# Kernel tuning notes

Measured on AMD Instinct MI355X. Metric: run time of the kernel, lower is better.

Reference implementation:

```python
import jax, jax.numpy as jnp
import numpy as np

N, E = 50000, 800000
IN_CH, N_HID, OUT_CH = 128, 256, 128
DROPOUT_P = 0.5


def gcn_conv(x, src, dst, ew, W, b, num_nodes):
    # PyG GCNConv with edge_weight: symmetric normalization with self-loops.
    loop = jnp.arange(num_nodes)
    s = jnp.concatenate([src, loop])
    d = jnp.concatenate([dst, loop])
    w = jnp.concatenate([ew, jnp.ones((num_nodes,), ew.dtype)])
    deg = jax.ops.segment_sum(w, d, num_segments=num_nodes)  # [N]
    dinv = jnp.where(deg > 0, jax.lax.rsqrt(deg), 0.0)
    norm = dinv[s] * w * dinv[d]                             # [E+N]
    h = x @ W                                                # [N, out]
    msg = h[s] * norm[:, None]                               # [E+N, out]
    out = jax.ops.segment_sum(msg, d, num_segments=num_nodes)
    return out + b


def setup_inputs() -> dict:
    key = jax.random.key(0)
    ks = jax.random.split(key, 8)
    x = jax.random.normal(ks[0], (N, IN_CH), dtype=jnp.float32)
    edge_index = jax.random.randint(ks[1], (2, E), 0, N, dtype=jnp.int64)
    weight = jax.random.uniform(ks[2], (E,), dtype=jnp.float32)
    # GCNConv params (glorot weights, zero bias)
    s1 = (6.0 / (IN_CH + N_HID)) ** 0.5
    s2 = (6.0 / (N_HID + OUT_CH)) ** 0.5
    W1 = jax.random.uniform(ks[3], (IN_CH, N_HID), jnp.float32, -s1, s1)
    b1 = jnp.zeros((N_HID,), jnp.float32)
    W2 = jax.random.uniform(ks[4], (N_HID, OUT_CH), jnp.float32, -s2, s2)
    b2 = jnp.zeros((OUT_CH,), jnp.float32)
    return {"x": x, "edge_index": edge_index, "weight": weight,
            "W1": W1, "b1": b1, "W2": W2, "b2": b2}


def reference(x, edge_index, weight, W1, b1, W2, b2):
    src, dst = edge_index[0], edge_index[1]
    h = jax.nn.relu(gcn_conv(x, src, dst, weight, W1, b1, N))
    # F.dropout(x, p) with training=True (torch default); fixed key for determinism
    keep = jax.random.bernoulli(jax.random.key(42), 1.0 - DROPOUT_P, h.shape)
    h = jnp.where(keep, h / (1.0 - DROPOUT_P), 0.0)
    return gcn_conv(h, src, dst, weight, W2, b2, N)
```

## Files before the change

kernel.cpp:

```cpp
#include <hip/hip_runtime.h>
#include <hip/hip_bf16.h>
#include <cstdint>

#define INCH 128
#define NHID 256
#define OUTCH 128
#define CAP 64

typedef unsigned short u16;
typedef unsigned long long u64;
typedef __attribute__((ext_vector_type(8))) short s8v;
typedef __attribute__((ext_vector_type(4))) float f4v;

__device__ __forceinline__ u16 tob(float a) {
    unsigned u = __float_as_uint(a);
    return (u16)((u + 0x7fffu + ((u >> 16) & 1u)) >> 16);
}

__device__ __forceinline__ void bsplit(float a, u16& hi, u16& lo) {
    unsigned u = __float_as_uint(a);
    unsigned r = (u + 0x7fffu + ((u >> 16) & 1u)) >> 16;
    hi = (u16)r;
    float res = a - __uint_as_float(r << 16);
    lo = tob(res);
}

__device__ __forceinline__ unsigned rotl32(unsigned x, int d) {
    return (x << d) | (x >> (32 - d));
}

__device__ __forceinline__ void threefry2x32(unsigned k0, unsigned k1,
                                             unsigned x0, unsigned x1,
                                             unsigned& o0, unsigned& o1) {
    unsigned ks2 = k0 ^ k1 ^ 0x1BD11BDAu;
#define TF_R(r) { x0 += x1; x1 = rotl32(x1, (r)); x1 ^= x0; }
    x0 += k0; x1 += k1;
    TF_R(13) TF_R(15) TF_R(26) TF_R(6)
    x0 += k1; x1 += ks2 + 1u;
    TF_R(17) TF_R(29) TF_R(16) TF_R(24)
    x0 += ks2; x1 += k0 + 2u;
    TF_R(13) TF_R(15) TF_R(26) TF_R(6)
    x0 += k0; x1 += k1 + 3u;
    TF_R(17) TF_R(29) TF_R(16) TF_R(24)
    x0 += k1; x1 += ks2 + 4u;
    TF_R(13) TF_R(15) TF_R(26) TF_R(6)
    x0 += ks2; x1 += k0 + 5u;
#undef TF_R
    o0 = x0; o1 = x1;
}

__global__ void k_zero64(u64* packed, int N) {
    int i = blockIdx.x * blockDim.x + threadIdx.x;
    if (i < N) packed[i] = 0ull;
}

__global__ void k_fill64(const int* __restrict__ src, const int* __restrict__ dst,
                         const float* __restrict__ w, u64* packed,
                         unsigned* __restrict__ buck, int E) {
    int e = blockIdx.x * blockDim.x + threadIdx.x;
    if (e < E) {
        int d = dst[e];
        float wv = w[e];
        u64 a = (1ull << 32) | (u64)__float2uint_rn(wv * 16777216.0f);
        u64 old = atomicAdd(&packed[d], a);
        unsigned pos = (unsigned)(old >> 32);
        if (pos < CAP)
            buck[(size_t)d * CAP + pos] = ((unsigned)tob(wv) << 16) | (unsigned)src[e];
    }
}

__global__ void k_dinv(const u64* __restrict__ packed, float* __restrict__ dinv, int N) {
    int i = blockIdx.x * blockDim.x + threadIdx.x;
    if (i < N) {
        float deg = 1.0f + (float)(unsigned)(packed[i] & 0xffffffffull) * (1.0f / 16777216.0f);
        dinv[i] = rsqrtf(deg);
    }
}

__global__ __launch_bounds__(256) void k_norm(unsigned* __restrict__ buck,
                                              const u64* __restrict__ packed,
                                              const float* __restrict__ dinv, int N) {
    int node = blockIdx.x * 8 + (threadIdx.x >> 5);
    int l = threadIdx.x & 31;
    if (node >= N) return;
    int c = min((int)(packed[node] >> 32), CAP);
    float dd = dinv[node];
    for (int p = l; p < c; p += 32) {
        unsigned u = buck[(size_t)node * CAP + p];
        unsigned s = u & 0xffffu;
        float wv = __uint_as_float(u & 0xffff0000u);
        float v = dinv[s] * wv * dd;
        buck[(size_t)node * CAP + p] = ((unsigned)tob(v) << 16) | s;
    }
}

__global__ __launch_bounds__(256) void k_prep(const float4* __restrict__ x,
                                              uint4* __restrict__ xb,
                                              unsigned* __restrict__ mask,
                                              const float* __restrict__ W1,
                                              u16* __restrict__ w1h, u16* __restrict__ w1l,
                                              const float* __restrict__ W2,
                                              u16* __restrict__ w2h, u16* __restrict__ w2l,
                                              int n8, int nwords) {
    int i = blockIdx.x * 256 + threadIdx.x;
    if (i < n8) {
        float4 a = x[i * 2], b = x[i * 2 + 1];
        uint4 o;
        o.x = (unsigned)tob(a.x) | ((unsigned)tob(a.y) << 16);
        o.y = (unsigned)tob(a.z) | ((unsigned)tob(a.w) << 16);
        o.z = (unsigned)tob(b.x) | ((unsigned)tob(b.y) << 16);
        o.w = (unsigned)tob(b.z) | ((unsigned)tob(b.w) << 16);
        xb[i] = o;
    }
    if (i < nwords) {
        unsigned base = (unsigned)i * 32u;
        unsigned m = 0;
#pragma unroll
        for (int b = 0; b < 32; ++b) {
            unsigned o0, o1;
            threefry2x32(0u, 42u, 0u, base + (unsigned)b, o0, o1);
            m |= ((((o0 ^ o1) >> 31) ^ 1u) & 1u) << b;
        }
        mask[i] = m;
    }
    if (i < INCH * NHID) {
        int k = i / NHID, n = i % NHID;
        u16 hi, lo;
        bsplit(W1[i], hi, lo);
        w1h[(size_t)n * INCH + k] = hi;
        w1l[(size_t)n * INCH + k] = lo;
    }
    if (i < NHID * OUTCH) {
        int k = i / OUTCH, n = i % OUTCH;
        u16 hi, lo;
        bsplit(W2[i], hi, lo);
        w2h[(size_t)n * NHID + k] = hi;
        w2l[(size_t)n * NHID + k] = lo;
    }
}

template <int BM, int BN, int MODE>
__global__ __launch_bounds__(256) void gemm_mfma(
    const u16* __restrict__ Ah, const u16* __restrict__ Al,
    const u16* __restrict__ Bh, const u16* __restrict__ Bl,
    const float* __restrict__ bias, const unsigned* __restrict__ mask,
    const float* __restrict__ dinv,
    u16* __restrict__ Ch, u16* __restrict__ Cl,
    u16* __restrict__ Cb, float* __restrict__ Sp,
    int M, int Ntot, int K) {
    constexpr int WN = BN / 2;
    constexpr int MFRAG = BM / 32;
    constexpr int NFRAG = WN / 16;
    __shared__ u16 Alh[BM][40], All[BM][40];
    __shared__ u16 Blh[BN][40], Bll[BN][40];

    const int tid = threadIdx.x;
    const int lane = tid & 63;
    const int w = tid >> 6;
    const int wm = (w >> 1) * (BM / 2);
    const int wn = (w & 1) * WN;
    const int l15 = lane & 15;
    const int kh = lane >> 4;
    const int row0 = blockIdx.y * BM;
    const int col0 = blockIdx.x * BN;

    f4v acc[MFRAG][NFRAG];
#pragma unroll
    for (int f = 0; f < MFRAG; ++f)
#pragma unroll
        for (int g = 0; g < NFRAG; ++g) acc[f][g] = (f4v){0.f, 0.f, 0.f, 0.f};

    for (int k0 = 0; k0 < K; k0 += 32) {
#pragma unroll
        for (int c = tid; c < BM * 4; c += 256) {
            int m = c >> 2, ko = (c & 3) * 8;
            int gm = row0 + m;
            uint4 vh = make_uint4(0, 0, 0, 0), vl = make_uint4(0, 0, 0, 0);
            if (gm < M) {
                size_t gi = (size_t)gm * K + k0 + ko;
                vh = *reinterpret_cast<const uint4*>(&Ah[gi]);
                vl = *reinterpret_cast<const uint4*>(&Al[gi]);
            }
            *reinterpret_cast<uint4*>(&Alh[m][ko]) = vh;
            *reinterpret_cast<uint4*>(&All[m][ko]) = vl;
        }
#pragma unroll
        for (int c = tid; c < BN * 4; c += 256) {
            int n = c >> 2, ko = (c & 3) * 8;
            size_t gi = (size_t)(col0 + n) * K + k0 + ko;
            *reinterpret_cast<uint4*>(&Blh[n][ko]) = *reinterpret_cast<const uint4*>(&Bh[gi]);
            *reinterpret_cast<uint4*>(&Bll[n][ko]) = *reinterpret_cast<const uint4*>(&Bl[gi]);
        }
        __syncthreads();

        s8v afh[MFRAG], afl[MFRAG], bfh[NFRAG], bfl[NFRAG];
#pragma unroll
        for (int f = 0; f < MFRAG; ++f) {
            afh[f] = *reinterpret_cast<const s8v*>(&Alh[wm + f * 16 + l15][kh * 8]);
            afl[f] = *reinterpret_cast<const s8v*>(&All[wm + f * 16 + l15][kh * 8]);
        }
#pragma unroll
        for (int g = 0; g < NFRAG; ++g) {
            bfh[g] = *reinterpret_cast<const s8v*>(&Blh[wn + g * 16 + l15][kh * 8]);
            bfl[g] = *reinterpret_cast<const s8v*>(&Bll[wn + g * 16 + l15][kh * 8]);
        }
#pragma unroll
        for (int f = 0; f < MFRAG; ++f)
#pragma unroll
            for (int g = 0; g < NFRAG; ++g) {
                acc[f][g] = __builtin_amdgcn_mfma_f32_16x16x32_bf16(afl[f], bfh[g], acc[f][g], 0, 0, 0);
                acc[f][g] = __builtin_amdgcn_mfma_f32_16x16x32_bf16(afh[f], bfl[g], acc[f][g], 0, 0, 0);
                acc[f][g] = __builtin_amdgcn_mfma_f32_16x16x32_bf16(afh[f], bfh[g], acc[f][g], 0, 0, 0);
            }
        __syncthreads();
    }

#pragma unroll
    for (int f = 0; f < MFRAG; ++f) {
#pragma unroll
        for (int g = 0; g < NFRAG; ++g) {
#pragma unroll
            for (int r = 0; r < 4; ++r) {
                int gr = row0 + wm + f * 16 + kh * 4 + r;
                if (gr >= M) continue;
                int gc = col0 + wn + g * 16 + l15;
                float v = acc[f][g][r];
                if (MODE == 0) {
                    v = fmaxf(v + bias[gc], 0.f);
                    unsigned j = (unsigned)gr * (unsigned)Ntot + (unsigned)gc;
                    unsigned keep = (mask[j >> 5] >> (j & 31u)) & 1u;
                    v = keep ? v * 2.f : 0.f;
                    u16 hi, lo;
                    bsplit(v, hi, lo);
                    Ch[(size_t)gr * Ntot + gc] = hi;
                    Cl[(size_t)gr * Ntot + gc] = lo;
                } else {
                    float d = dinv[gr];
                    Cb[(size_t)gr * Ntot + gc] = tob(v);
                    Sp[(size_t)gr * Ntot + gc] = fmaf(v, d * d, bias[gc]);
                }
            }
        }
    }
}

template <bool SPLIT>
__global__ __launch_bounds__(256) void k_agg_q(const uint4* __restrict__ gb,
                                               const float4* __restrict__ selfs,
                                               const float* __restrict__ dinv,
                                               const u64* __restrict__ packed,
                                               const unsigned* __restrict__ buck,
                                               uint4* __restrict__ outh,
                                               uint4* __restrict__ outl,
                                               float4* __restrict__ outf,
                                               int N, int q) {
    int node = blockIdx.x * 64 + (threadIdx.x >> 2);
    int l = threadIdx.x & 3;
    if (node >= N) return;
    const int q4 = q * 4 + l;
    const int q8 = q * 8 + l * 2;
    float4 s0 = selfs[(size_t)node * 32 + q8];
    float4 s1 = selfs[(size_t)node * 32 + q8 + 1];
    float a0, a1, a2, a3, a4, a5, a6, a7;
    if (SPLIT) {
        float d = dinv[node], sc = d * d;
        a0 = s0.x * sc; a1 = s0.y * sc; a2 = s0.z * sc; a3 = s0.w * sc;
        a4 = s1.x * sc; a5 = s1.y * sc; a6 = s1.z * sc; a7 = s1.w * sc;
    } else {
        a0 = s0.x; a1 = s0.y; a2 = s0.z; a3 = s0.w;
        a4 = s1.x; a5 = s1.y; a6 = s1.z; a7 = s1.w;
    }
#define ACCB(gv, ev) { float v = __uint_as_float((ev) & 0xffff0000u); \
    a0 = fmaf(__uint_as_float((gv).x << 16), v, a0); \
    a1 = fmaf(__uint_as_float((gv).x & 0xffff0000u), v, a1); \
    a2 = fmaf(__uint_as_float((gv).y << 16), v, a2); \
    a3 = fmaf(__uint_as_float((gv).y & 0xffff0000u), v, a3); \
    a4 = fmaf(__uint_as_float((gv).z << 16), v, a4); \
    a5 = fmaf(__uint_as_float((gv).z & 0xffff0000u), v, a5); \
    a6 = fmaf(__uint_as_float((gv).w << 16), v, a6); \
    a7 = fmaf(__uint_as_float((gv).w & 0xffff0000u), v, a7); }
    int c = min((int)(packed[node] >> 32), CAP);
    const unsigned* row = buck + (size_t)node * CAP;
    int p = 0;
    for (; p + 8 <= c; p += 8) {
        unsigned e0 = row[p + 0], e1 = row[p + 1], e2 = row[p + 2], e3 = row[p + 3];
        unsigned e4 = row[p + 4], e5 = row[p + 5], e6 = row[p + 6], e7 = row[p + 7];
        uint4 g0 = gb[(size_t)(e0 & 0xffffu) * 16 + q4];
        uint4 g1 = gb[(size_t)(e1 & 0xffffu) * 16 + q4];
        uint4 g2 = gb[(size_t)(e2 & 0xffffu) * 16 + q4];
        uint4 g3 = gb[(size_t)(e3 & 0xffffu) * 16 + q4];
        uint4 g4 = gb[(size_t)(e4 & 0xffffu) * 16 + q4];
        uint4 g5 = gb[(size_t)(e5 & 0xffffu) * 16 + q4];
        uint4 g6 = gb[(size_t)(e6 & 0xffffu) * 16 + q4];
        uint4 g7 = gb[(size_t)(e7 & 0xffffu) * 16 + q4];
        ACCB(g0, e0) ACCB(g1, e1) ACCB(g2, e2) ACCB(g3, e3)
        ACCB(g4, e4) ACCB(g5, e5) ACCB(g6, e6) ACCB(g7, e7)
    }
    for (; p < c; ++p) {
        unsigned e = row[p];
        uint4 g = gb[(size_t)(e & 0xffffu) * 16 + q4];
        ACCB(g, e)
    }
#undef ACCB
    if (SPLIT) {
        u16 h[8], lo[8];
        bsplit(a0, h[0], lo[0]); bsplit(a1, h[1], lo[1]);
        bsplit(a2, h[2], lo[2]); bsplit(a3, h[3], lo[3]);
        bsplit(a4, h[4], lo[4]); bsplit(a5, h[5], lo[5]);
        bsplit(a6, h[6], lo[6]); bsplit(a7, h[7], lo[7]);
        uint4 oh, ol;
        oh.x = (unsigned)h[0] | ((unsigned)h[1] << 16);
        oh.y = (unsigned)h[2] | ((unsigned)h[3] << 16);
        oh.z = (unsigned)h[4] | ((unsigned)h[5] << 16);
        oh.w = (unsigned)h[6] | ((unsigned)h[7] << 16);
        ol.x = (unsigned)lo[0] | ((unsigned)lo[1] << 16);
        ol.y = (unsigned)lo[2] | ((unsigned)lo[3] << 16);
        ol.z = (unsigned)lo[4] | ((unsigned)lo[5] << 16);
        ol.w = (unsigned)lo[6] | ((unsigned)lo[7] << 16);
        outh[(size_t)node * 16 + q4] = oh;
        outl[(size_t)node * 16 + q4] = ol;
    } else {
        outf[(size_t)node * 32 + q8]     = make_float4(a0, a1, a2, a3);
        outf[(size_t)node * 32 + q8 + 1] = make_float4(a4, a5, a6, a7);
    }
}

extern "C" void kernel_launch(void* const* d_in, const int* in_sizes, int n_in,
                              void* d_out, int out_size, void* d_ws, size_t ws_size,
                              hipStream_t stream) {
    (void)n_in; (void)out_size; (void)ws_size;
    const float* x  = (const float*)d_in[0];
    const int*   ei = (const int*)d_in[1];
    const float* w  = (const float*)d_in[2];
    const float* W1 = (const float*)d_in[3];
    const float* b1 = (const float*)d_in[4];
    const float* W2 = (const float*)d_in[5];
    const float* b2 = (const float*)d_in[6];
    float* out = (float*)d_out;

    int N = in_sizes[0] / INCH;
    int E = in_sizes[1] / 2;
    const int* src = ei;
    const int* dst = ei + E;

    char* ws = (char*)d_ws;
    size_t off = 0;
    auto alloc = [&](size_t bytes) -> char* {
        size_t p = (off + 255) & ~(size_t)255;
        off = p + bytes;
        return ws + p;
    };
    u64*      packed = (u64*)     alloc((size_t)N * 8);
    float*    dinv   = (float*)   alloc((size_t)N * 4);
    unsigned* buck   = (unsigned*)alloc((size_t)N * CAP * 4);
    unsigned* mask   = (unsigned*)alloc((size_t)N * NHID / 8);
    u16*      xb     = (u16*)     alloc((size_t)N * INCH * 2);
    u16*      axh    = (u16*)     alloc((size_t)N * INCH * 2);
    u16*      axl    = (u16*)     alloc((size_t)N * INCH * 2);
    u16*      hdh    = (u16*)     alloc((size_t)N * NHID * 2);
    u16*      hdl    = (u16*)     alloc((size_t)N * NHID * 2);
    u16*      w1h    = (u16*)     alloc((size_t)INCH * NHID * 2);
    u16*      w1l    = (u16*)     alloc((size_t)INCH * NHID * 2);
    u16*      w2h    = (u16*)     alloc((size_t)NHID * OUTCH * 2);
    u16*      w2l    = (u16*)     alloc((size_t)NHID * OUTCH * 2);
    u16*      g2b    = xb;
    float*    sp     = (float*)axh;

    int nb = (N + 255) / 256;
    int eb = (E + 255) / 256;
    int n8 = N * INCH / 8;
    int nwords = N * NHID / 32;
    int hb = (N + 7) / 8;
    int qb = (N + 63) / 64;

    k_zero64<<<nb, 256, 0, stream>>>(packed, N);
    k_fill64<<<eb, 256, 0, stream>>>(src, dst, w, packed, buck, E);
    k_dinv<<<nb, 256, 0, stream>>>(packed, dinv, N);
    k_norm<<<hb, 256, 0, stream>>>(buck, packed, dinv, N);
    k_prep<<<(n8 + 255) / 256, 256, 0, stream>>>((const float4*)x, (uint4*)xb, mask,
                                                 W1, w1h, w1l, W2, w2h, w2l, n8, nwords);

    for (int q = 0; q < 4; ++q)
        k_agg_q<true><<<qb, 256, 0, stream>>>((const uint4*)xb, (const float4*)x, dinv,
                                              packed, buck, (uint4*)axh, (uint4*)axl,
                                              nullptr, N, q);
    dim3 gg1(NHID / 128, (N + 63) / 64);
    gemm_mfma<64, 128, 0><<<gg1, 256, 0, stream>>>(axh, axl, w1h, w1l, b1, mask, nullptr,
                                                   hdh, hdl, nullptr, nullptr,
                                                   N, NHID, INCH);
    dim3 gg2(OUTCH / 64, (N + 63) / 64);
    gemm_mfma<64, 64, 1><<<gg2, 256, 0, stream>>>(hdh, hdl, w2h, w2l, b2, nullptr, dinv,
                                                  nullptr, nullptr, g2b, sp,
                                                  N, OUTCH, NHID);
    for (int q = 0; q < 4; ++q)
        k_agg_q<false><<<qb, 256, 0, stream>>>((const uint4*)g2b, (const float4*)sp, nullptr,
                                               packed, buck, nullptr, nullptr,
                                               (float4*)out, N, q);
}
```

Baseline: 364.1 us.

## Register-prefetch GEMM tiles and aggregate all feature quarters in one launch

```diff
diff --git a/kernel.cpp b/kernel.cpp
--- a/kernel.cpp
+++ b/kernel.cpp
@@ -151,6 +151,8 @@
     constexpr int WN = BN / 2;
     constexpr int MFRAG = BM / 32;
     constexpr int NFRAG = WN / 16;
+    constexpr int AV = BM * 4 / 256;
+    constexpr int BV = BN * 4 / 256;
     __shared__ u16 Alh[BM][40], All[BM][40];
     __shared__ u16 Blh[BN][40], Bll[BN][40];
 
@@ -170,29 +172,48 @@
 #pragma unroll
         for (int g = 0; g < NFRAG; ++g) acc[f][g] = (f4v){0.f, 0.f, 0.f, 0.f};
 
-    for (int k0 = 0; k0 < K; k0 += 32) {
-#pragma unroll
-        for (int c = tid; c < BM * 4; c += 256) {
+    uint4 pah[AV], pal[AV], pbh[BV], pbl[BV];
+
+    auto loadg = [&](int k0) {
+#pragma unroll
+        for (int v = 0; v < AV; ++v) {
+            int c = tid + v * 256;
             int m = c >> 2, ko = (c & 3) * 8;
             int gm = row0 + m;
-            uint4 vh = make_uint4(0, 0, 0, 0), vl = make_uint4(0, 0, 0, 0);
+            pah[v] = make_uint4(0, 0, 0, 0);
+            pal[v] = make_uint4(0, 0, 0, 0);
             if (gm < M) {
                 size_t gi = (size_t)gm * K + k0 + ko;
-                vh = *reinterpret_cast<const uint4*>(&Ah[gi]);
-                vl = *reinterpret_cast<const uint4*>(&Al[gi]);
+                pah[v] = *reinterpret_cast<const uint4*>(&Ah[gi]);
+                pal[v] = *reinterpret_cast<const uint4*>(&Al[gi]);
             }
-            *reinterpret_cast<uint4*>(&Alh[m][ko]) = vh;
-            *reinterpret_cast<uint4*>(&All[m][ko]) = vl;
-        }
-#pragma unroll
-        for (int c = tid; c < BN * 4; c += 256) {
+        }
+#pragma unroll
+        for (int v = 0; v < BV; ++v) {
+            int c = tid + v * 256;
             int n = c >> 2, ko = (c & 3) * 8;
             size_t gi = (size_t)(col0 + n) * K + k0 + ko;
-            *reinterpret_cast<uint4*>(&Blh[n][ko]) = *reinterpret_cast<const uint4*>(&Bh[gi]);
-            *reinterpret_cast<uint4*>(&Bll[n][ko]) = *reinterpret_cast<const uint4*>(&Bl[gi]);
-        }
-        __syncthreads();
-
+            pbh[v] = *reinterpret_cast<const uint4*>(&Bh[gi]);
+            pbl[v] = *reinterpret_cast<const uint4*>(&Bl[gi]);
+        }
+    };
+    auto store_lds = [&]() {
+#pragma unroll
+        for (int v = 0; v < AV; ++v) {
+            int c = tid + v * 256;
+            int m = c >> 2, ko = (c & 3) * 8;
+            *reinterpret_cast<uint4*>(&Alh[m][ko]) = pah[v];
+            *reinterpret_cast<uint4*>(&All[m][ko]) = pal[v];
+        }
+#pragma unroll
+        for (int v = 0; v < BV; ++v) {
+            int c = tid + v * 256;
+            int n = c >> 2, ko = (c & 3) * 8;
+            *reinterpret_cast<uint4*>(&Blh[n][ko]) = pbh[v];
+            *reinterpret_cast<uint4*>(&Bll[n][ko]) = pbl[v];
+        }
+    };
+    auto compute = [&]() {
         s8v afh[MFRAG], afl[MFRAG], bfh[NFRAG], bfl[NFRAG];
 #pragma unroll
         for (int f = 0; f < MFRAG; ++f) {
@@ -212,8 +233,19 @@
                 acc[f][g] = __builtin_amdgcn_mfma_f32_16x16x32_bf16(afh[f], bfl[g], acc[f][g], 0, 0, 0);
                 acc[f][g] = __builtin_amdgcn_mfma_f32_16x16x32_bf16(afh[f], bfh[g], acc[f][g], 0, 0, 0);
             }
+    };
+
+    loadg(0);
+    store_lds();
+    __syncthreads();
+    for (int k0 = 32; k0 < K; k0 += 32) {
+        loadg(k0);
+        compute();
         __syncthreads();
-    }
+        store_lds();
+        __syncthreads();
+    }
+    compute();
 
 #pragma unroll
     for (int f = 0; f < MFRAG; ++f) {
@@ -245,22 +277,19 @@
 }
 
 template <bool SPLIT>
-__global__ __launch_bounds__(256) void k_agg_q(const uint4* __restrict__ gb,
+__global__ __launch_bounds__(256) void k_agg_b(const uint4* __restrict__ gb,
                                                const float4* __restrict__ selfs,
                                                const float* __restrict__ dinv,
                                                const u64* __restrict__ packed,
                                                const unsigned* __restrict__ buck,
                                                uint4* __restrict__ outh,
                                                uint4* __restrict__ outl,
-                                               float4* __restrict__ outf,
-                                               int N, int q) {
-    int node = blockIdx.x * 64 + (threadIdx.x >> 2);
-    int l = threadIdx.x & 3;
+                                               float4* __restrict__ outf, int N) {
+    int node = blockIdx.x * 16 + (threadIdx.x >> 4);
+    int l = threadIdx.x & 15;
     if (node >= N) return;
-    const int q4 = q * 4 + l;
-    const int q8 = q * 8 + l * 2;
-    float4 s0 = selfs[(size_t)node * 32 + q8];
-    float4 s1 = selfs[(size_t)node * 32 + q8 + 1];
+    float4 s0 = selfs[(size_t)node * 32 + l * 2];
+    float4 s1 = selfs[(size_t)node * 32 + l * 2 + 1];
     float a0, a1, a2, a3, a4, a5, a6, a7;
     if (SPLIT) {
         float d = dinv[node], sc = d * d;
@@ -285,20 +314,20 @@
     for (; p + 8 <= c; p += 8) {
         unsigned e0 = row[p + 0], e1 = row[p + 1], e2 = row[p + 2], e3 = row[p + 3];
         unsigned e4 = row[p + 4], e5 = row[p + 5], e6 = row[p + 6], e7 = row[p + 7];
-        uint4 g0 = gb[(size_t)(e0 & 0xffffu) * 16 + q4];
-        uint4 g1 = gb[(size_t)(e1 & 0xffffu) * 16 + q4];
-        uint4 g2 = gb[(size_t)(e2 & 0xffffu) * 16 + q4];
-        uint4 g3 = gb[(size_t)(e3 & 0xffffu) * 16 + q4];
-        uint4 g4 = gb[(size_t)(e4 & 0xffffu) * 16 + q4];
-        uint4 g5 = gb[(size_t)(e5 & 0xffffu) * 16 + q4];
-        uint4 g6 = gb[(size_t)(e6 & 0xffffu) * 16 + q4];
-        uint4 g7 = gb[(size_t)(e7 & 0xffffu) * 16 + q4];
+        uint4 g0 = gb[(size_t)(e0 & 0xffffu) * 16 + l];
+        uint4 g1 = gb[(size_t)(e1 & 0xffffu) * 16 + l];
+        uint4 g2 = gb[(size_t)(e2 & 0xffffu) * 16 + l];
+        uint4 g3 = gb[(size_t)(e3 & 0xffffu) * 16 + l];
+        uint4 g4 = gb[(size_t)(e4 & 0xffffu) * 16 + l];
+        uint4 g5 = gb[(size_t)(e5 & 0xffffu) * 16 + l];
+        uint4 g6 = gb[(size_t)(e6 & 0xffffu) * 16 + l];
+        uint4 g7 = gb[(size_t)(e7 & 0xffffu) * 16 + l];
         ACCB(g0, e0) ACCB(g1, e1) ACCB(g2, e2) ACCB(g3, e3)
         ACCB(g4, e4) ACCB(g5, e5) ACCB(g6, e6) ACCB(g7, e7)
     }
     for (; p < c; ++p) {
         unsigned e = row[p];
-        uint4 g = gb[(size_t)(e & 0xffffu) * 16 + q4];
+        uint4 g = gb[(size_t)(e & 0xffffu) * 16 + l];
         ACCB(g, e)
     }
 #undef ACCB
@@ -317,11 +346,11 @@
         ol.y = (unsigned)lo[2] | ((unsigned)lo[3] << 16);
         ol.z = (unsigned)lo[4] | ((unsigned)lo[5] << 16);
         ol.w = (unsigned)lo[6] | ((unsigned)lo[7] << 16);
-        outh[(size_t)node * 16 + q4] = oh;
-        outl[(size_t)node * 16 + q4] = ol;
+        outh[(size_t)node * 16 + l] = oh;
+        outl[(size_t)node * 16 + l] = ol;
     } else {
-        outf[(size_t)node * 32 + q8]     = make_float4(a0, a1, a2, a3);
-        outf[(size_t)node * 32 + q8 + 1] = make_float4(a4, a5, a6, a7);
+        outf[(size_t)node * 32 + l * 2]     = make_float4(a0, a1, a2, a3);
+        outf[(size_t)node * 32 + l * 2 + 1] = make_float4(a4, a5, a6, a7);
     }
 }
 
@@ -371,7 +400,7 @@
     int n8 = N * INCH / 8;
     int nwords = N * NHID / 32;
     int hb = (N + 7) / 8;
-    int qb = (N + 63) / 64;
+    int ab = (N + 15) / 16;
 
     k_zero64<<<nb, 256, 0, stream>>>(packed, N);
     k_fill64<<<eb, 256, 0, stream>>>(src, dst, w, packed, buck, E);
@@ -380,10 +409,9 @@
     k_prep<<<(n8 + 255) / 256, 256, 0, stream>>>((const float4*)x, (uint4*)xb, mask,
                                                  W1, w1h, w1l, W2, w2h, w2l, n8, nwords);
 
-    for (int q = 0; q < 4; ++q)
-        k_agg_q<true><<<qb, 256, 0, stream>>>((const uint4*)xb, (const float4*)x, dinv,
-                                              packed, buck, (uint4*)axh, (uint4*)axl,
-                                              nullptr, N, q);
+    k_agg_b<true><<<ab, 256, 0, stream>>>((const uint4*)xb, (const float4*)x, dinv,
+                                          packed, buck, (uint4*)axh, (uint4*)axl,
+                                          nullptr, N);
     dim3 gg1(NHID / 128, (N + 63) / 64);
     gemm_mfma<64, 128, 0><<<gg1, 256, 0, stream>>>(axh, axl, w1h, w1l, b1, mask, nullptr,
                                                    hdh, hdl, nullptr, nullptr,
@@ -392,8 +420,7 @@
     gemm_mfma<64, 64, 1><<<gg2, 256, 0, stream>>>(hdh, hdl, w2h, w2l, b2, nullptr, dinv,
                                                   nullptr, nullptr, g2b, sp,
                                                   N, OUTCH, NHID);
-    for (int q = 0; q < 4; ++q)
-        k_agg_q<false><<<qb, 256, 0, stream>>>((const uint4*)g2b, (const float4*)sp, nullptr,
-                                               packed, buck, nullptr, nullptr,
-                                               (float4*)out, N, q);
-}
+    k_agg_b<false><<<ab, 256, 0, stream>>>((const uint4*)g2b, (const float4*)sp, nullptr,
+                                           packed, buck, nullptr, nullptr,
+                                           (float4*)out, N);
+}
```

After: 332.3 us. 1.1x faster.
